# Optimization experiments

Measured on AMD Instinct MI355X. Metric: run time of the kernel, lower is better.

## Reference

```python
import jax, jax.numpy as jnp
import numpy as np

DZ = 16
DX = 16
T = 256
K = 2 * T  # quad-form slots: slot 0 = prior, odd = integrated obs terms, even = transition terms
LOG2PI = float(np.log(2.0 * np.pi))


def setup_inputs() -> dict:
    key = jax.random.key(0)
    ks = jax.random.split(key, 20)

    def spd(k, d, s=0.5):
        L = jax.random.normal(k, (d, d))
        return s * (L @ L.T) / d + jnp.eye(d)

    sc = 1.0 / np.sqrt(DZ)
    return {
        "observations": jax.random.normal(ks[0], (T, DX)),
        "p_prior_mean": 0.1 * jax.random.normal(ks[1], (DZ,)),
        "p_prior_cov": spd(ks[2], DZ),
        "p_trans_w": 0.7 * sc * jax.random.normal(ks[3], (DZ, DZ)),
        "p_trans_b": 0.1 * jax.random.normal(ks[4], (DZ,)),
        "p_trans_cov": spd(ks[5], DZ),
        "p_em_w": sc * jax.random.normal(ks[6], (DX, DZ)),
        "p_em_b": 0.1 * jax.random.normal(ks[7], (DX,)),
        "p_em_cov": spd(ks[8], DX),
        "q_prior_mean": 0.1 * jax.random.normal(ks[9], (DZ,)),
        "q_prior_cov": spd(ks[10], DZ),
        "q_trans_w": 0.7 * sc * jax.random.normal(ks[11], (DZ, DZ)),
        "q_trans_b": 0.1 * jax.random.normal(ks[12], (DZ,)),
        "q_trans_cov": spd(ks[13], DZ),
        "q_em_w": sc * jax.random.normal(ks[14], (DX, DZ)),
        "q_em_b": 0.1 * jax.random.normal(ks[15], (DX,)),
        "q_em_cov": spd(ks[16], DX),
    }


def reference(observations, p_prior_mean, p_prior_cov, p_trans_w, p_trans_b, p_trans_cov,
              p_em_w, p_em_b, p_em_cov, q_prior_mean, q_prior_cov, q_trans_w, q_trans_b,
              q_trans_cov, q_em_w, q_em_b, q_em_cov):
    dz, dx = DZ, DX
    I = jnp.eye(dz, dtype=observations.dtype)

    def cterm(dim, det):  # -0.5*(d*log(2pi) + log det)
        return -0.5 * (dim * LOG2PI + jnp.log(det))

    p_tr_prec = jnp.linalg.inv(p_trans_cov)
    p_tr_det = jnp.linalg.det(p_trans_cov)
    p_em_prec = jnp.linalg.inv(p_em_cov)
    p_em_det = jnp.linalg.det(p_em_cov)
    q_tr_prec = jnp.linalg.inv(q_trans_cov)
    Om_obs = -0.5 * p_em_prec   # Omega of every observation term (linear-Gaussian emission)
    Om_tr = -0.5 * p_tr_prec    # Omega of every transition quad form

    def kupdate(m_pred, P_pred, y):  # Kalman measurement update under q
        S = q_em_w @ P_pred @ q_em_w.T + q_em_cov
        Kg = P_pred @ q_em_w.T @ jnp.linalg.inv(S)
        m = m_pred + Kg @ (y - q_em_w @ m_pred - q_em_b)
        P = (I - Kg @ q_em_w) @ P_pred
        return m, P

    # init: filtering + V
    m_f, P_f = kupdate(q_prior_mean, q_prior_cov, observations[0])
    const = cterm(dz, jnp.linalg.det(p_prior_cov)) + cterm(dx, p_em_det)
    As = jnp.zeros((K, dz, dz), observations.dtype).at[0].set(I)
    bs = jnp.zeros((K, dz), observations.dtype).at[0].set(-p_prior_mean)
    # static Omega stack (inactive slots have A=0,b=0 so they contribute exactly 0)
    odd = (jnp.arange(K) % 2 == 1)[:, None, None]
    Om = jnp.where(odd, Om_obs[None], Om_tr[None])
    Om = Om.at[0].set(-0.5 * jnp.linalg.inv(p_prior_cov))
    pend_b = p_em_b - observations[0]  # pending obs term: (Om_obs, p_em_w, pend_b)

    def step(carry, inp):
        As, bs, pend_b, m_f, P_f, const = carry
        y, t = inp
        # backward kernel from current filtering
        P_prec = jnp.linalg.inv(P_f)
        bprec = q_trans_w.T @ q_tr_prec @ q_trans_w + P_prec
        bcov = jnp.linalg.inv(bprec)
        cm = q_trans_w.T @ q_tr_prec
        B = bcov @ cm
        a = bcov @ (P_prec @ m_f - cm @ q_trans_b)
        # integrate all existing quad forms under backward: trace(Om A bcov A^T), A<-A@B, b<-A@a+b
        ACA = jnp.einsum('kij,jl,kml->kim', As, bcov, As)
        const = const + jnp.einsum('kij,kji->', Om, ACA)
        bs = jnp.einsum('kij,j->ki', As, a) + bs
        As = jnp.einsum('kij,jl->kil', As, B)
        # integrate pending observation term, append at slot 2t-1
        const = const + jnp.trace(Om_obs @ p_em_w @ bcov @ p_em_w.T)
        As = As.at[2 * t - 1].set(p_em_w @ B)
        bs = bs.at[2 * t - 1].set(p_em_w @ a + pend_b)
        # per-step constants
        const = (const + cterm(dx, p_em_det) + cterm(dz, p_tr_det)
                 - cterm(dz, jnp.linalg.det(bcov)) + 0.5 * dz
                 - 0.5 * jnp.trace(p_tr_prec @ p_trans_w @ bcov @ p_trans_w.T))
        # transition quad form at slot 2t
        As = As.at[2 * t].set(p_trans_w @ B - I)
        bs = bs.at[2 * t].set(p_trans_w @ a + p_trans_b)
        pend_b = p_em_b - y
        # Kalman filter step under q
        m_pred = q_trans_w @ m_f + q_trans_b
        P_pred = q_trans_w @ P_f @ q_trans_w.T + q_trans_cov
        m_f, P_f = kupdate(m_pred, P_pred, y)
        return (As, bs, pend_b, m_f, P_f, const), None

    ts = jnp.arange(1, T)
    (As, bs, pend_b, m_f, P_f, const), _ = jax.lax.scan(
        step, (As, bs, pend_b, m_f, P_f, const), (observations[1:], ts))

    const = const - cterm(dz, jnp.linalg.det(P_f))
    # expectation of quad forms under filtering (NOTE: trace(Om A P A), no final
    # transpose -- faithful to the source's _expect_quad_form_under_filtering)
    tr = jnp.einsum('kij,kjl,lm,kmi->', Om, As, P_f, As)
    u = jnp.einsum('kij,j->ki', As, m_f) + bs
    ev = jnp.einsum('ki,kij,kj->', u, Om, u)
    # pending observation term under filtering (same formula)
    up = p_em_w @ m_f + pend_b
    tr_p = jnp.trace(Om_obs @ p_em_w @ P_f @ p_em_w)
    ev_p = up @ Om_obs @ up
    return const + tr + ev + tr_p + ev_p + 0.5 * dz
```

## Files before the change

kernel.cpp:

```cpp
#include <hip/hip_runtime.h>
#include <cmath>

#define L2PI 1.8378770664093453f
#define CT16 (16.f * L2PI)

__device__ __align__(16) float g_Gstore[255 * 256];
__device__ float g_Pff[256], g_Om0[256], g_Omo[256], g_Omt[256], g_Ginf[256];
__device__ float g_partial, g_acc;
__device__ int g_tb;
__device__ unsigned g_cnt;

__device__ __forceinline__ float dAB(const float* A, const float* B, int i, int j) {
  float s = 0.f;
#pragma unroll
  for (int k = 0; k < 16; ++k) s = fmaf(A[i * 16 + k], B[k * 16 + j], s);
  return s;
}
__device__ __forceinline__ float dATB(const float* A, const float* B, int i, int j) {
  float s = 0.f;
#pragma unroll
  for (int k = 0; k < 16; ++k) s = fmaf(A[k * 16 + i], B[k * 16 + j], s);
  return s;
}
__device__ __forceinline__ float dABT(const float* A, const float* B, int i, int j) {
  float s = 0.f;
#pragma unroll
  for (int k = 0; k < 16; ++k) s = fmaf(A[i * 16 + k], B[j * 16 + k], s);
  return s;
}
__device__ __forceinline__ float mv(const float* M, const float* v, int r) {
  float s = 0.f;
#pragma unroll
  for (int k = 0; k < 16; ++k) s = fmaf(M[r * 16 + k], v[k], s);
  return s;
}
__device__ __forceinline__ float mvT(const float* M, const float* v, int r) {
  float s = 0.f;
#pragma unroll
  for (int k = 0; k < 16; ++k) s = fmaf(M[k * 16 + r], v[k], s);
  return s;
}
__device__ __forceinline__ float wave_sum(float v) {
#pragma unroll
  for (int off = 32; off; off >>= 1) v += __shfl_down(v, off);
  return v;
}
__device__ __forceinline__ float wave_max(float v) {
#pragma unroll
  for (int off = 32; off; off >>= 1) v = fmaxf(v, __shfl_down(v, off));
  return v;
}
__device__ __forceinline__ float rl(float v, int l) {
  return __int_as_float(__builtin_amdgcn_readlane(__float_as_int(v), l));
}

__device__ __forceinline__ float reg_gj_core(const float* __restrict__ src,
                                             float aI[4]) {
  const int wl = threadIdx.x & 63;
  const int col = wl & 15, rg = wl >> 4;
  float aA[4];
#pragma unroll
  for (int q = 0; q < 4; ++q) {
    const int r = rg + 4 * q;
    aA[q] = src[r * 16 + col];
    aI[q] = (r == col) ? 1.f : 0.f;
  }
  float det = 1.f;
#pragma unroll
  for (int k = 0; k < 16; ++k) {
    const int kq = k >> 2, kr = k & 3;
    const float piv = rl(aA[kq], (kr << 4) | k);
    det *= piv;
    const float rp = 1.f / piv;
    const float pA = __shfl(aA[kq], (kr << 4) | col);
    const float pI = __shfl(aI[kq], (kr << 4) | col);
    float f[4];
    f[0] = __shfl(aA[0], (rg << 4) | k);
    f[1] = __shfl(aA[1], (rg << 4) | k);
    f[2] = __shfl(aA[2], (rg << 4) | k);
    f[3] = __shfl(aA[3], (rg << 4) | k);
#pragma unroll
    for (int q = 0; q < 4; ++q) {
      const float tq = f[q] * rp;
      const float nA = fmaf(-tq, pA, aA[q]);
      const float nI = fmaf(-tq, pI, aI[q]);
      if (q == kq) {
        const bool isp = (rg == kr);
        aA[q] = isp ? pA * rp : nA;
        aI[q] = isp ? pI * rp : nI;
      } else {
        aA[q] = nA;
        aI[q] = nI;
      }
    }
  }
  return det;
}

__device__ __forceinline__ float reg_gj_inv(const float* __restrict__ src,
                                            float* __restrict__ dst) {
  const int wl = threadIdx.x & 63;
  const int col = wl & 15, rg = wl >> 4;
  float aI[4];
  const float det = reg_gj_core(src, aI);
#pragma unroll
  for (int q = 0; q < 4; ++q) dst[(rg + 4 * q) * 16 + col] = aI[q];
  return det;
}

template <int MODE>
__device__ __forceinline__ float gj_inv_mul(const float* __restrict__ src,
                                            const float* __restrict__ Bm,
                                            float* __restrict__ dst) {
  const int wl = threadIdx.x & 63;
  const int col = wl & 15, rg = wl >> 4;
  float aI[4];
  const float det = reg_gj_core(src, aI);
  float part[16];
#pragma unroll
  for (int ii = 0; ii < 16; ++ii) {
    float s = 0.f;
#pragma unroll
    for (int q = 0; q < 4; ++q) {
      const int k = rg + 4 * q;
      s = fmaf(MODE == 0 ? Bm[k * 16 + ii] : Bm[ii * 16 + k], aI[q], s);
    }
    part[ii] = s;
  }
#pragma unroll
  for (int ii = 0; ii < 16; ++ii) {
    part[ii] += __shfl_xor(part[ii], 16);
    part[ii] += __shfl_xor(part[ii], 32);
  }
  if (rg == 0) {
    dst[0 * 16 + col] = part[0];  dst[1 * 16 + col] = part[1];
    dst[2 * 16 + col] = part[2];  dst[3 * 16 + col] = part[3];
  } else if (rg == 1) {
    dst[4 * 16 + col] = part[4];  dst[5 * 16 + col] = part[5];
    dst[6 * 16 + col] = part[6];  dst[7 * 16 + col] = part[7];
  } else if (rg == 2) {
    dst[8 * 16 + col] = part[8];  dst[9 * 16 + col] = part[9];
    dst[10 * 16 + col] = part[10]; dst[11 * 16 + col] = part[11];
  } else {
    dst[12 * 16 + col] = part[12]; dst[13 * 16 + col] = part[13];
    dst[14 * 16 + col] = part[14]; dst[15 * 16 + col] = part[15];
  }
  return det;
}

__global__ void __launch_bounds__(256)
lgq_fwd(const float* __restrict__ obs,
        const float* __restrict__ ppm, const float* __restrict__ ppc,
        const float* __restrict__ ptw, const float* __restrict__ ptb,
        const float* __restrict__ ptc, const float* __restrict__ pew,
        const float* __restrict__ peb, const float* __restrict__ pec,
        const float* __restrict__ qpm, const float* __restrict__ qpc,
        const float* __restrict__ qtw, const float* __restrict__ qtb,
        const float* __restrict__ qtc, const float* __restrict__ qew,
        const float* __restrict__ qeb, const float* __restrict__ qec) {
  const int e = threadIdx.x;
  const int i = e >> 4, j = e & 15;
  const int wid = e >> 6;
  const int lane = e & 63;

  __shared__ float W[256], Qm[256], Hm[256], Rm[256], Em[256], Pwm[256];
  __shared__ float HW[256], QHt[256], HQH[256], TmpB[256];
  __shared__ float Om0[256], Omo[256], Omt[256], Fo[256], Ft[256], Nm[256], EOm[256];
  __shared__ float Sm[256], Pf[256];
  __shared__ float WP[256], U[256], Ppred[256], Smat[256], PHt[256];
  __shared__ float Pi[256], Si[256], Gm[256], Kgm[256], Mm[256], T1m[256], NGm[256];
  __shared__ float sObs[256 * 16];
  __shared__ float detPArr[256], detSArr[256], d3all[256];
  __shared__ float uB1[252 * 16], pB1[252 * 16], pC1[252 * 16];
  __shared__ float mfs1[252 * 16], rvs1[252 * 16];
  __shared__ float mf[16], mfN[16], rv[16], pb[16], bqv[16], bemv[16], pbemv[16],
      ptbv[16];
  __shared__ float w2[16], q2[16], mpred[16], av[16], hv[16];
  __shared__ float EOpb[16], resid[16], tv1[16], tv2[16], Opf[16];
  __shared__ float ca[16], mca[16], nca[16], c1[16], cg1[16], qc[16], epbm[16];
  __shared__ float red[4], red2[4], red3[4], dets[6];
  __shared__ float sc_const, sc_c, ctb, sh_cstep;
  __shared__ float ld_pprior, ld_ptr, ld_pem, ld_Q, ld_R, ld_qprior, ld_Pf;
  __shared__ float sh_detS, sh_tstep_inf;
  __shared__ int sh_frozen;

  W[e] = qtw[e]; Qm[e] = qtc[e]; Hm[e] = qew[e]; Rm[e] = qec[e];
  Em[e] = pew[e]; Pwm[e] = ptw[e];
  {
    const float4* o4 = (const float4*)obs;
    float4* s4 = (float4*)sObs;
#pragma unroll
    for (int q = 0; q < 4; ++q) s4[e + 256 * q] = o4[e + 256 * q];
  }
  if (e < 16) { bqv[e] = qtb[e]; bemv[e] = qeb[e]; pbemv[e] = peb[e]; ptbv[e] = ptb[e]; }
  if (e == 0) { sh_frozen = 0; g_acc = 0.f; g_cnt = 0u; }
  __syncthreads();
  HW[e] = dAB(Hm, W, i, j);
  TmpB[e] = dAB(Hm, Qm, i, j);
  __syncthreads();
  HQH[e] = dABT(TmpB, Hm, i, j) + Rm[e];
  QHt[e] = TmpB[j * 16 + i];
  __syncthreads();
  if (wid == 0) {
    float d0 = reg_gj_inv(ppc, Pi);
    float d1 = reg_gj_inv(ptc, Si);
    if (e == 0) { dets[0] = d0; dets[1] = d1; }
  } else if (wid == 1) {
    float d2 = reg_gj_inv(pec, Gm);
    float d3 = reg_gj_inv(qtc, Kgm);
    if (e == 64) { dets[2] = d2; dets[3] = d3; }
  } else if (wid == 2) {
    float d4 = reg_gj_inv(qec, T1m);
    float d5 = reg_gj_inv(qpc, NGm);
    if (e == 128) { dets[4] = d4; dets[5] = d5; }
  }
  __syncthreads();
  Om0[e] = -0.5f * Pi[e];
  Omt[e] = -0.5f * Si[e];
  Omo[e] = -0.5f * Gm[e];
  g_Om0[e] = Om0[e]; g_Omo[e] = Omo[e]; g_Omt[e] = Omt[e];
  Sm[e] = Om0[e];
  TmpB[e] = -0.5f * dAB(Gm, Em, i, j);
  Nm[e] = -0.5f * dAB(Si, Pwm, i, j);
  EOm[e] = -0.5f * dATB(Em, Gm, i, j);
  if (e == 0) {
    ld_pprior = logf(dets[0]); ld_ptr = logf(dets[1]); ld_pem = logf(dets[2]);
    ld_Q = logf(dets[3]); ld_R = logf(dets[4]); ld_qprior = logf(dets[5]);
  }
  __syncthreads();
  Fo[e] = dATB(Em, TmpB, i, j);
  Ft[e] = dATB(Pwm, Nm, i, j);
  if (e < 16) w2[e] = mvT(Nm, ptbv, e);
  else if (e < 32) q2[e - 16] = mv(Omt, ptbv, e - 16);
  else if (e < 48) rv[e - 32] = -mv(Om0, ppm, e - 32);
  else if (e < 64) pb[e - 48] = pbemv[e - 48] - sObs[e - 48];
  {
    const int rr = e & 15, tg = e >> 4;
#pragma unroll
    for (int it = 0; it < 16; ++it) {
      const int tt = it * 16 + tg;
      float s = 0.f;
#pragma unroll
      for (int k = 0; k < 16; ++k)
        s = fmaf(Omo[rr * 16 + k], pbemv[k] - sObs[tt * 16 + k], s);
      s *= (pbemv[rr] - sObs[tt * 16 + rr]);
      s += __shfl_xor(s, 1); s += __shfl_xor(s, 2);
      s += __shfl_xor(s, 4); s += __shfl_xor(s, 8);
      if (rr == 0) d3all[tt] = s;
    }
  }
  __syncthreads();
  if (e == 0) {
    float s = 0.f, ct = 0.f;
    for (int k = 0; k < 16; ++k) { s = fmaf(ppm[k], rv[k], s); ct = fmaf(ptbv[k], q2[k], ct); }
    sc_c = -s;
    ctb = ct;
    sc_const = -0.5f * (CT16 + ld_pprior) - 0.5f * (CT16 + ld_pem);
    sh_cstep = 8.f - 0.5f * CT16 - 0.5f * (ld_pem + ld_ptr);
  }
  if (e < 16) mpred[e] = qpm[e];
  TmpB[e] = dAB(Hm, qpc, i, j);
  __syncthreads();
  Smat[e] = dABT(TmpB, Hm, i, j) + Rm[e];
  if (e < 16) resid[e] = sObs[e] - bemv[e] - mv(Hm, mpred, e);
  __syncthreads();
  if (wid == 0) {
    float d = reg_gj_inv(Smat, Si);
    if (e == 0) sh_detS = d;
  }
  __syncthreads();
  Kgm[e] = dATB(TmpB, Si, i, j);
  if (e == 0) ld_Pf = ld_qprior + ld_R - logf(sh_detS);
  __syncthreads();
  Pf[e] = qpc[e] - dAB(Kgm, TmpB, i, j);
  if (e < 16) { mf[e] = mpred[e] + mv(Kgm, resid, e); mfN[e] = mf[e]; }
  __syncthreads();

  float d1acc = 0.f, tacc = 0.f, fd2 = 0.f, facc = 0.f;
  int t = 1;
  for (; t < 256; ++t) {
    const float* y = sObs + t * 16;
    WP[e] = dAB(W, Pf, i, j);
    U[e] = dAB(HW, Pf, i, j);
    if (t > 1) {
      const float sN = dATB(Gm, T1m, i, j) - NGm[j * 16 + i] - NGm[e] + Omt[e];
      const float sd = fabsf(sN - Sm[e]);
      Sm[e] = sN;
      const float vm = wave_max(sd);
      if (lane == 0) red3[wid] = vm;
      d1acc = fmaf(Mm[e] * av[i], av[j], d1acc);
      if (e < 16) {
        float s = -q2[e];
#pragma unroll
        for (int k = 0; k < 16; ++k) {
          s = fmaf(T1m[k * 16 + e], av[k], s);
          s = fmaf(Gm[k * 16 + e], hv[k], s);
          s = fmaf(-Nm[e * 16 + k], av[k], s);
        }
        rv[e] = s;
      } else if (e < 32) {
        fd2 = fmaf(av[e - 16], hv[e - 16], fd2);
        mf[e - 16] = mfN[e - 16];
      } else if (e < 48) {
        mpred[e - 32] = bqv[e - 32] + mv(W, mfN, e - 32);
      }
    } else {
      if (e < 16) mpred[e] = bqv[e] + mv(W, mf, e);
    }
    __syncthreads();
    Ppred[e] = dABT(WP, W, i, j) + Qm[e];
    Smat[e] = dABT(U, HW, i, j) + HQH[e];
    PHt[e] = dABT(WP, HW, i, j) + QHt[e];
    if (e < 16) resid[e] = y[e] - bemv[e] - mv(Hm, mpred, e);
    if (e == 0 && t >= 5) {
      const float pfd = fmaxf(fmaxf(red2[0], red2[1]), fmaxf(red2[2], red2[3]));
      const float sdm = fmaxf(fmaxf(red3[0], red3[1]), fmaxf(red3[2], red3[3]));
      if (pfd < 3e-3f && sdm < 3e-2f) sh_frozen = 1;
    }
    __syncthreads();
    if (sh_frozen) break;
    if (wid == 0) {
      const float d = gj_inv_mul<0>(Ppred, WP, Gm);
      if (e == 0) detPArr[t] = d;
    } else if (wid == 1) {
      const float d = gj_inv_mul<1>(Smat, PHt, Kgm);
      if (e == 64) detSArr[t] = d;
    } else if (wid == 2) {
      const int wl = e & 63;
#pragma unroll
      for (int q = 0; q < 4; ++q) { const int x = wl + 64 * q; Mm[x] = Sm[x] + Fo[x] + Ft[x]; }
      if (wl < 16) EOpb[wl] = mv(EOm, pb, wl);
    }
    __syncthreads();
    {
      const float bc = Pf[e] - dAB(Gm, WP, i, j);
      tacc = fmaf(Mm[e], bc, tacc);
      const float pfN = Ppred[e] - dABT(Kgm, PHt, i, j);
      const float df = fabsf(pfN - Pf[e]);
      Pf[e] = pfN;
      const float vm = wave_max(df);
      if (lane == 0) red2[wid] = vm;
    }
    T1m[e] = dAB(Mm, Gm, i, j);
    NGm[e] = dAB(Nm, Gm, i, j);
    g_Gstore[(t - 1) * 256 + e] = Gm[e];
    if (e < 16) av[e] = mf[e] - mv(Gm, mpred, e);
    else if (e < 32) mfN[e - 16] = mpred[e - 16] + mv(Kgm, resid, e - 16);
    else if (e < 48) hv[e - 32] = rv[e - 32] + EOpb[e - 32] + w2[e - 32];
    else if (e < 64) pb[e - 48] = pbemv[e - 48] - y[e - 48];
    __syncthreads();
  }

  const int tb = t;
  if (sh_frozen) {
    const int NT = 256 - tb;
    const int AA = NT & ~3;
    const int r16 = e & 15, kslot = e >> 4;
    T1m[e] = dAB(Kgm, Hm, i, j);
    NGm[e] = ((i == j) ? 1.f : 0.f) - dAB(Gm, W, i, j);
    Mm[e] = Sm[e] + Fo[e] + Ft[e];
    if (e < 16) ca[e] = -mv(Gm, bqv, e);
    else if (e < 32) epbm[e - 16] = mv(EOm, pbemv, e - 16);
    __syncthreads();
    Smat[e] = W[e] - dAB(T1m, W, i, j);
    Pi[e] = dAB(Mm, NGm, i, j);
    Si[e] = dAB(Nm, NGm, i, j);
    {
      const float bcf = Pf[e] - dAB(Gm, WP, i, j);
      const float v = wave_sum(Mm[e] * bcf);
      if (lane == 0) red[wid] = v;
    }
    if (e < 16) mca[e] = mv(Mm, ca, e);
    else if (e < 32) nca[e - 16] = mv(Nm, ca, e - 16);
    else if (e < 48) {
      const int r = e - 32;
      c1[r] = bqv[r] - mv(T1m, bqv, r) - mv(Kgm, bemv, r);
    }
    __syncthreads();
    U[e] = dATB(Gm, Pi, i, j) - Si[e];
    Ppred[e] = dATB(Gm, EOm, i, j);
    Fo[e] = dAB(Smat, Smat, i, j);
    HW[e] = dAB(Gm, Gm, i, j);
    if (e < 16) {
      float s = 0.f;
#pragma unroll
      for (int k = 0; k < 16; ++k)
        s = fmaf(Gm[k * 16 + e], w2[k] + mca[k] + epbm[k], s);
      cg1[e] = s - nca[e] - q2[e];
    } else if (e < 32) {
      const int r = e - 16;
      qc[r] = mca[r] + 2.f * w2[r] + 2.f * epbm[r];
    } else if (e < 48) {
      mfs1[e - 32] = mf[e - 32];
    } else if (e < 64) {
      rvs1[e - 48] = rv[e - 48];
    }
    if (e == 0) sh_tstep_inf = red[0] + red[1] + red[2] + red[3];
    {
      float kgrow[16];
#pragma unroll
      for (int k2 = 0; k2 < 16; ++k2) kgrow[k2] = Kgm[r16 * 16 + k2];
      const float c1r = c1[r16];
      for (int k = 1 + kslot; k <= NT; k += 16) {
        const float* yc = sObs + (tb - 1 + k) * 16;
        float s = c1r;
#pragma unroll
        for (int k2 = 0; k2 < 16; ++k2) s = fmaf(kgrow[k2], yc[k2], s);
        uB1[k * 16 + r16] = s;
      }
    }
    __syncthreads();
    Ft[e] = dAB(Fo, Fo, i, j);
    QHt[e] = dAB(HW, HW, i, j);
    {
      float a1row[16];
#pragma unroll
      for (int k2 = 0; k2 < 16; ++k2) a1row[k2] = Smat[r16 * 16 + k2];
      for (int k = 2 + kslot; k <= NT; k += 16) {
        const float* up = uB1 + (k - 1) * 16;
        float s = uB1[k * 16 + r16];
#pragma unroll
        for (int k2 = 0; k2 < 16; ++k2) s = fmaf(a1row[k2], up[k2], s);
        pB1[k * 16 + r16] = s;
      }
    }
    __syncthreads();
    {
      float a2row[16];
#pragma unroll
      for (int k2 = 0; k2 < 16; ++k2) a2row[k2] = Fo[r16 * 16 + k2];
      for (int k = 4 + kslot; k <= NT; k += 16) {
        const float* pp = pB1 + (k - 2) * 16;
        float s = pB1[k * 16 + r16];
#pragma unroll
        for (int k2 = 0; k2 < 16; ++k2) s = fmaf(a2row[k2], pp[k2], s);
        pC1[k * 16 + r16] = s;
      }
    }
    __syncthreads();
    if (wid == 0 && AA >= 4) {
      const int r = lane & 15;
      float a4row[16];
#pragma unroll
      for (int k2 = 0; k2 < 16; ++k2) a4row[k2] = Ft[r * 16 + k2];
      float x = mf[r];
      float d0 = pC1[4 * 16 + r];
      float d1 = (AA >= 8) ? pC1[8 * 16 + r] : 0.f;
      for (int k = 4; k <= AA; k += 4) {
        const float d2 = (k + 8 <= AA) ? pC1[(k + 8) * 16 + r] : 0.f;
        float s0 = d0, s1 = 0.f, s2 = 0.f, s3 = 0.f;
#pragma unroll
        for (int k2 = 0; k2 < 16; k2 += 4) {
          s0 = fmaf(a4row[k2],     rl(x, k2),     s0);
          s1 = fmaf(a4row[k2 + 1], rl(x, k2 + 1), s1);
          s2 = fmaf(a4row[k2 + 2], rl(x, k2 + 2), s2);
          s3 = fmaf(a4row[k2 + 3], rl(x, k2 + 3), s3);
        }
        x = (s0 + s1) + (s2 + s3);
        if (lane < 16) mfs1[k * 16 + r] = x;
        d0 = d1; d1 = d2;
      }
    }
    __syncthreads();
    {
      float a1row[16], a2row[16];
#pragma unroll
      for (int k2 = 0; k2 < 16; ++k2) {
        a1row[k2] = Smat[r16 * 16 + k2];
        a2row[k2] = Fo[r16 * 16 + k2];
      }
      for (int a = 4 * kslot; a <= NT; a += 64) {
        const float* mfp = mfs1 + a * 16;
        if (a + 1 <= NT) {
          float s = uB1[(a + 1) * 16 + r16];
#pragma unroll
          for (int k2 = 0; k2 < 16; ++k2) s = fmaf(a1row[k2], mfp[k2], s);
          mfs1[(a + 1) * 16 + r16] = s;
        }
        if (a + 2 <= NT) {
          float s = pB1[(a + 2) * 16 + r16];
#pragma unroll
          for (int k2 = 0; k2 < 16; ++k2) s = fmaf(a2row[k2], mfp[k2], s);
          mfs1[(a + 2) * 16 + r16] = s;
        }
      }
    }
    __syncthreads();
    {
      float a2row[16];
#pragma unroll
      for (int k2 = 0; k2 < 16; ++k2) a2row[k2] = Fo[r16 * 16 + k2];
      for (int a = 4 * kslot; a <= NT; a += 64) {
        if (a + 3 <= NT) {
          const float* mfp = mfs1 + (a + 1) * 16;
          float s = pB1[(a + 3) * 16 + r16];
#pragma unroll
          for (int k2 = 0; k2 < 16; ++k2) s = fmaf(a2row[k2], mfp[k2], s);
          mfs1[(a + 3) * 16 + r16] = s;
        }
      }
    }
    __syncthreads();
    {
      float b1row[16], georow[16];
#pragma unroll
      for (int k2 = 0; k2 < 16; ++k2) {
        b1row[k2] = U[r16 * 16 + k2];
        georow[k2] = Ppred[r16 * 16 + k2];
      }
      const float cg1r = cg1[r16];
      for (int k = 1 + kslot; k <= NT; k += 16) {
        const float* mfp = mfs1 + (k - 1) * 16;
        const float* yp = sObs + (tb - 2 + k) * 16;
        float s = cg1r;
#pragma unroll
        for (int k2 = 0; k2 < 16; ++k2) {
          s = fmaf(b1row[k2], mfp[k2], s);
          s = fmaf(-georow[k2], yp[k2], s);
        }
        uB1[k * 16 + r16] = s;
      }
    }
    if (e < 16) { mf[e] = mfs1[NT * 16 + e]; pb[e] = pbemv[e] - sObs[255 * 16 + e]; }
    __syncthreads();
    {
      float gtrow[16];
#pragma unroll
      for (int k2 = 0; k2 < 16; ++k2) gtrow[k2] = Gm[k2 * 16 + r16];
      for (int k = 2 + kslot; k <= NT; k += 16) {
        const float* wp = uB1 + (k - 1) * 16;
        float s = uB1[k * 16 + r16];
#pragma unroll
        for (int k2 = 0; k2 < 16; ++k2) s = fmaf(gtrow[k2], wp[k2], s);
        pB1[k * 16 + r16] = s;
      }
    }
    __syncthreads();
    {
      float gt2row[16];
#pragma unroll
      for (int k2 = 0; k2 < 16; ++k2) gt2row[k2] = HW[k2 * 16 + r16];
      for (int k = 4 + kslot; k <= NT; k += 16) {
        const float* wp = pB1 + (k - 2) * 16;
        float s = pB1[k * 16 + r16];
#pragma unroll
        for (int k2 = 0; k2 < 16; ++k2) s = fmaf(gt2row[k2], wp[k2], s);
        pC1[k * 16 + r16] = s;
      }
    }
    __syncthreads();
    if (wid == 0 && AA >= 4) {
      const int r = lane & 15;
      float g4row[16];
#pragma unroll
      for (int k2 = 0; k2 < 16; ++k2) g4row[k2] = QHt[k2 * 16 + r];
      float x = rv[r];
      float d0 = pC1[4 * 16 + r];
      float d1 = (AA >= 8) ? pC1[8 * 16 + r] : 0.f;
      for (int k = 4; k <= AA; k += 4) {
        const float d2 = (k + 8 <= AA) ? pC1[(k + 8) * 16 + r] : 0.f;
        float s0 = d0, s1 = 0.f, s2 = 0.f, s3 = 0.f;
#pragma unroll
        for (int k2 = 0; k2 < 16; k2 += 4) {
          s0 = fmaf(g4row[k2],     rl(x, k2),     s0);
          s1 = fmaf(g4row[k2 + 1], rl(x, k2 + 1), s1);
          s2 = fmaf(g4row[k2 + 2], rl(x, k2 + 2), s2);
          s3 = fmaf(g4row[k2 + 3], rl(x, k2 + 3), s3);
        }
        x = (s0 + s1) + (s2 + s3);
        if (lane < 16) rvs1[k * 16 + r] = x;
        d0 = d1; d1 = d2;
      }
    }
    __syncthreads();
    {
      float gtrow[16], gt2row[16];
#pragma unroll
      for (int k2 = 0; k2 < 16; ++k2) {
        gtrow[k2] = Gm[k2 * 16 + r16];
        gt2row[k2] = HW[k2 * 16 + r16];
      }
      for (int a = 4 * kslot; a <= NT; a += 64) {
        const float* rp = rvs1 + a * 16;
        if (a + 1 <= NT) {
          float s = uB1[(a + 1) * 16 + r16];
#pragma unroll
          for (int k2 = 0; k2 < 16; ++k2) s = fmaf(gtrow[k2], rp[k2], s);
          rvs1[(a + 1) * 16 + r16] = s;
        }
        if (a + 2 <= NT) {
          float s = pB1[(a + 2) * 16 + r16];
#pragma unroll
          for (int k2 = 0; k2 < 16; ++k2) s = fmaf(gt2row[k2], rp[k2], s);
          rvs1[(a + 2) * 16 + r16] = s;
        }
      }
    }
    __syncthreads();
    {
      float gt2row[16];
#pragma unroll
      for (int k2 = 0; k2 < 16; ++k2) gt2row[k2] = HW[k2 * 16 + r16];
      for (int a = 4 * kslot; a <= NT; a += 64) {
        if (a + 3 <= NT) {
          const float* rp = rvs1 + (a + 1) * 16;
          float s = pB1[(a + 3) * 16 + r16];
#pragma unroll
          for (int k2 = 0; k2 < 16; ++k2) s = fmaf(gt2row[k2], rp[k2], s);
          rvs1[(a + 3) * 16 + r16] = s;
        }
      }
    }
    __syncthreads();
    {
      float avrow[16], mavrow[16], eorow[16];
#pragma unroll
      for (int k2 = 0; k2 < 16; ++k2) {
        avrow[k2] = NGm[r16 * 16 + k2];
        mavrow[k2] = Pi[r16 * 16 + k2];
        eorow[k2] = EOm[r16 * 16 + k2];
      }
      const float car = ca[r16], qcr = qc[r16];
      for (int k = 1 + kslot; k <= NT; k += 16) {
        const float* mfp = mfs1 + (k - 1) * 16;
        const float* yp = sObs + (tb - 2 + k) * 16;
        float avr = car, qr = qcr + 2.f * rvs1[(k - 1) * 16 + r16];
#pragma unroll
        for (int k2 = 0; k2 < 16; ++k2) {
          avr = fmaf(avrow[k2], mfp[k2], avr);
          qr = fmaf(mavrow[k2], mfp[k2], qr);
          qr = fmaf(-2.f * eorow[k2], yp[k2], qr);
        }
        facc = fmaf(avr, qr, facc);
      }
    }
    if (e < 16) rv[e] = rvs1[NT * 16 + e];
    __syncthreads();
  } else {
    const float sN = dATB(Gm, T1m, i, j) - NGm[j * 16 + i] - NGm[e] + Omt[e];
    Sm[e] = sN;
    d1acc = fmaf(Mm[e] * av[i], av[j], d1acc);
    if (e < 16) {
      float s = -q2[e];
#pragma unroll
      for (int k = 0; k < 16; ++k) {
        s = fmaf(T1m[k * 16 + e], av[k], s);
        s = fmaf(Gm[k * 16 + e], hv[k], s);
        s = fmaf(-Nm[e * 16 + k], av[k], s);
      }
      rv[e] = s;
    } else if (e < 32) {
      fd2 = fmaf(av[e - 16], hv[e - 16], fd2);
      mf[e - 16] = mfN[e - 16];
    }
    __syncthreads();
  }

  const int n = tb - 1;
  if (e >= 1 && e <= n) {
    detPArr[e] = logf(detPArr[e]);
    detSArr[e] = logf(detSArr[e]);
  }
  {
    const float vA = d1acc + 2.f * fd2 + facc;
    const float vB = tacc;
    const float vC = (e < 255) ? d3all[e] : 0.f;
    const float sA = wave_sum(vA);
    const float sB = wave_sum(vB);
    const float sC = wave_sum(vC);
    if (lane == 0) { red[wid] = sA; red2[wid] = sB; red3[wid] = sC; }
  }
  __syncthreads();
  if (e == 0) {
    const float dsum = red[0] + red[1] + red[2] + red[3];
    const float tsum = red2[0] + red2[1] + red2[2] + red2[3];
    const float d3tot = red3[0] + red3[1] + red3[2] + red3[3];
    float lpf = ld_Pf;
    float sum_ldb = 0.f, ldbl = 0.f;
    for (int s2 = 1; s2 <= n; ++s2) {
      ldbl = lpf + ld_Q - detPArr[s2];
      sum_ldb += ldbl;
      lpf = detPArr[s2] + ld_R - detSArr[s2];
    }
    float sc = sc_const + tsum + (float)n * sh_cstep + 0.5f * sum_ldb;
    if (tb < 256) sc += (float)(256 - tb) * (sh_tstep_inf + sh_cstep + 0.5f * ldbl);
    sc_const = sc;
    ld_Pf = lpf;
    sc_c += dsum + d3tot + 255.f * ctb;
  }
  __syncthreads();

  g_Pff[e] = Pf[e];
  g_Ginf[e] = Gm[e];
  if (e == 0) g_tb = tb;
  WP[e] = dAB(Pf, Em, i, j);
  if (e < 16) tv1[e] = mv(Sm, mf, e);
  else if (e < 32) tv2[e - 16] = pb[e - 16] + mv(Em, mf, e - 16);
  __syncthreads();
  {
    const float v = wave_sum(EOm[e] * WP[e]);
    if (lane == 0) red[wid] = v;
  }
  if (e < 16) Opf[e] = mv(Omo, tv2, e);
  __syncthreads();
  if (e == 0) {
    const float tr_p = red[0] + red[1] + red[2] + red[3];
    float ev1 = 0.f, ev2 = 0.f, evp = 0.f;
    for (int k = 0; k < 16; ++k) {
      ev1 = fmaf(mf[k], tv1[k], ev1);
      ev2 = fmaf(rv[k], mf[k], ev2);
      evp = fmaf(tv2[k], Opf[k], evp);
    }
    g_partial = sc_const + 0.5f * (CT16 + ld_Pf) + (ev1 + 2.f * ev2 + sc_c)
                + tr_p + evp + 8.f;
  }
}

__global__ void __launch_bounds__(256)
lgq_trace(const float* __restrict__ pew, const float* __restrict__ ptw,
          float* __restrict__ out) {
  const int e = threadIdx.x, i = e >> 4, j = e & 15, b = blockIdx.x;
  const int lane = e & 63, wid = e >> 6;
  __shared__ float Pfs[256], OmA[256], OmtS[256], EmS[256], PwS[256], GinfS[256];
  __shared__ float Xb[2][256], Bb[2][256];
  __shared__ float Sm1[256], Sf[256], A1[256], A2[256];
  __shared__ float T1v[256], NGv[256], Kxv[256], S2v[256];
  __shared__ float redt[4];
  int tb = g_tb;
  tb = (tb < 1) ? 1 : (tb > 256 ? 256 : tb);
  Pfs[e] = g_Pff[e];
  OmtS[e] = g_Omt[e];
  EmS[e] = pew[e];
  PwS[e] = ptw[e];
  GinfS[e] = g_Ginf[e];
  OmA[e] = (b == 0) ? g_Om0[e] : g_Omo[e];
  Xb[0][e] = (i == j) ? 1.f : 0.f;
  Bb[0][e] = g_Ginf[e];
  __syncthreads();
  int E = (b >= tb) ? (255 - b) : (256 - tb);
  int xc = 0, bc2 = 0;
  while (E) {
    Xb[xc ^ 1][e] = (E & 1) ? dAB(Xb[xc], Bb[bc2], i, j) : Xb[xc][e];
    if (E > 1) Bb[bc2 ^ 1][e] = dAB(Bb[bc2], Bb[bc2], i, j);
    __syncthreads();
    xc ^= 1; bc2 ^= 1;
    E >>= 1;
  }
  if (b >= tb) {
    Sf[e] = Xb[xc][e];
    Sm1[e] = dAB(GinfS, Xb[xc], i, j);
    __syncthreads();
  } else {
    int cur = xc;
    for (int s2 = tb - 1; s2 >= b + 1; --s2) {
      const float4* gr = (const float4*)(g_Gstore + (s2 - 1) * 256 + i * 16);
      const float4 a0 = gr[0], a1 = gr[1], a2 = gr[2], a3 = gr[3];
      const float* Xc = Xb[cur];
      float s = 0.f;
      s = fmaf(a0.x, Xc[0 * 16 + j], s);  s = fmaf(a0.y, Xc[1 * 16 + j], s);
      s = fmaf(a0.z, Xc[2 * 16 + j], s);  s = fmaf(a0.w, Xc[3 * 16 + j], s);
      s = fmaf(a1.x, Xc[4 * 16 + j], s);  s = fmaf(a1.y, Xc[5 * 16 + j], s);
      s = fmaf(a1.z, Xc[6 * 16 + j], s);  s = fmaf(a1.w, Xc[7 * 16 + j], s);
      s = fmaf(a2.x, Xc[8 * 16 + j], s);  s = fmaf(a2.y, Xc[9 * 16 + j], s);
      s = fmaf(a2.z, Xc[10 * 16 + j], s); s = fmaf(a2.w, Xc[11 * 16 + j], s);
      s = fmaf(a3.x, Xc[12 * 16 + j], s); s = fmaf(a3.y, Xc[13 * 16 + j], s);
      s = fmaf(a3.z, Xc[14 * 16 + j], s); s = fmaf(a3.w, Xc[15 * 16 + j], s);
      Xb[cur ^ 1][e] = s;
      __syncthreads();
      cur ^= 1;
    }
    Sf[e] = Xb[cur][e];
    if (b >= 1) {
      const float4* gr = (const float4*)(g_Gstore + (b - 1) * 256 + i * 16);
      const float4 a0 = gr[0], a1 = gr[1], a2 = gr[2], a3 = gr[3];
      const float* Xc = Xb[cur];
      float s = 0.f;
      s = fmaf(a0.x, Xc[0 * 16 + j], s);  s = fmaf(a0.y, Xc[1 * 16 + j], s);
      s = fmaf(a0.z, Xc[2 * 16 + j], s);  s = fmaf(a0.w, Xc[3 * 16 + j], s);
      s = fmaf(a1.x, Xc[4 * 16 + j], s);  s = fmaf(a1.y, Xc[5 * 16 + j], s);
      s = fmaf(a1.z, Xc[6 * 16 + j], s);  s = fmaf(a1.w, Xc[7 * 16 + j], s);
      s = fmaf(a2.x, Xc[8 * 16 + j], s);  s = fmaf(a2.y, Xc[9 * 16 + j], s);
      s = fmaf(a2.z, Xc[10 * 16 + j], s); s = fmaf(a2.w, Xc[11 * 16 + j], s);
      s = fmaf(a3.x, Xc[12 * 16 + j], s); s = fmaf(a3.y, Xc[13 * 16 + j], s);
      s = fmaf(a3.z, Xc[14 * 16 + j], s); s = fmaf(a3.w, Xc[15 * 16 + j], s);
      Sm1[e] = s;
    } else {
      Sm1[e] = Xb[cur][e];
    }
    __syncthreads();
  }
  if (b == 0) {
    A1[e] = Sm1[e];
    A2[e] = 0.f;
  } else {
    A1[e] = dAB(EmS, Sm1, i, j);
    A2[e] = dAB(PwS, Sm1, i, j) - Sf[e];
  }
  __syncthreads();
  T1v[e] = dAB(OmA, A1, i, j);
  NGv[e] = dAB(Pfs, A1, i, j);
  Kxv[e] = dAB(OmtS, A2, i, j);
  S2v[e] = dAB(Pfs, A2, i, j);
  __syncthreads();
  float val = T1v[e] * NGv[j * 16 + i] + Kxv[e] * S2v[j * 16 + i];
  val = wave_sum(val);
  if (lane == 0) redt[wid] = val;
  __syncthreads();
  if (e == 0) {
    atomicAdd(&g_acc, redt[0] + redt[1] + redt[2] + redt[3]);
    __threadfence();
    const unsigned o = atomicAdd(&g_cnt, 1u);
    if (o == 255u) {
      const float acc = atomicAdd(&g_acc, 0.f);
      out[0] = g_partial + acc;
    }
  }
}

extern "C" void kernel_launch(void* const* d_in, const int* in_sizes, int n_in,
                              void* d_out, int out_size, void* d_ws, size_t ws_size,
                              hipStream_t stream) {
  (void)in_sizes; (void)n_in; (void)out_size; (void)d_ws; (void)ws_size;
  lgq_fwd<<<dim3(1), dim3(256), 0, stream>>>(
      (const float*)d_in[0], (const float*)d_in[1], (const float*)d_in[2],
      (const float*)d_in[3], (const float*)d_in[4], (const float*)d_in[5],
      (const float*)d_in[6], (const float*)d_in[7], (const float*)d_in[8],
      (const float*)d_in[9], (const float*)d_in[10], (const float*)d_in[11],
      (const float*)d_in[12], (const float*)d_in[13], (const float*)d_in[14],
      (const float*)d_in[15], (const float*)d_in[16]);
  lgq_trace<<<dim3(256), dim3(256), 0, stream>>>((const float*)d_in[6],
                                                 (const float*)d_in[3],
                                                 (float*)d_out);
}
```

Before: 96.32 us.

## Keep transposed copies of matrices so 16x16 products read contiguous rows

Adds transposed shared-memory copies (WT, EmT, PwmT, GmT, T1mT, NGmT, TmpBT, NmT, WPT) and rewrites the dAB/dATB products as dABT, so each thread reads both operands along contiguous rows instead of strided columns. This is meant to reduce LDS bank conflicts and allow vectorised loads. The prior Kalman gain is now computed by the fused gj_inv_mul, which removes one barrier. The freeze check may now fire one step earlier (t>=4 instead of t>=5). The cost is extra LDS footprint and extra transposed stores on every iteration, and the earlier freeze could change results slightly.

```diff
diff --git a/kernel.cpp b/kernel.cpp
--- a/kernel.cpp
+++ b/kernel.cpp
@@ -32,12 +32,6 @@
   float s = 0.f;
 #pragma unroll
   for (int k = 0; k < 16; ++k) s = fmaf(M[r * 16 + k], v[k], s);
-  return s;
-}
-__device__ __forceinline__ float mvT(const float* M, const float* v, int r) {
-  float s = 0.f;
-#pragma unroll
-  for (int k = 0; k < 16; ++k) s = fmaf(M[k * 16 + r], v[k], s);
   return s;
 }
 __device__ __forceinline__ float wave_sum(float v) {
@@ -111,7 +105,8 @@
 template <int MODE>
 __device__ __forceinline__ float gj_inv_mul(const float* __restrict__ src,
                                             const float* __restrict__ Bm,
-                                            float* __restrict__ dst) {
+                                            float* __restrict__ dst,
+                                            float* __restrict__ dstT) {
   const int wl = threadIdx.x & 63;
   const int col = wl & 15, rg = wl >> 4;
   float aI[4];
@@ -135,6 +130,13 @@
   if (rg == 0) {
     dst[0 * 16 + col] = part[0];  dst[1 * 16 + col] = part[1];
     dst[2 * 16 + col] = part[2];  dst[3 * 16 + col] = part[3];
+    if (dstT) {
+      float4* p4 = (float4*)(dstT + col * 16);
+      p4[0] = make_float4(part[0], part[1], part[2], part[3]);
+      p4[1] = make_float4(part[4], part[5], part[6], part[7]);
+      p4[2] = make_float4(part[8], part[9], part[10], part[11]);
+      p4[3] = make_float4(part[12], part[13], part[14], part[15]);
+    }
   } else if (rg == 1) {
     dst[4 * 16 + col] = part[4];  dst[5 * 16 + col] = part[5];
     dst[6 * 16 + col] = part[6];  dst[7 * 16 + col] = part[7];
@@ -163,12 +165,15 @@
   const int wid = e >> 6;
   const int lane = e & 63;
 
-  __shared__ float W[256], Qm[256], Hm[256], Rm[256], Em[256], Pwm[256];
-  __shared__ float HW[256], QHt[256], HQH[256], TmpB[256];
-  __shared__ float Om0[256], Omo[256], Omt[256], Fo[256], Ft[256], Nm[256], EOm[256];
+  __shared__ float W[256], WT[256], Qm[256], Hm[256], Rm[256], Em[256], EmT[256],
+      PwmT[256];
+  __shared__ float HW[256], QHt[256], HQH[256], TmpB[256], TmpBT[256];
+  __shared__ float Om0[256], Omo[256], Omt[256], Fo[256], Ft[256], Nm[256],
+      NmT[256], EOm[256];
   __shared__ float Sm[256], Pf[256];
-  __shared__ float WP[256], U[256], Ppred[256], Smat[256], PHt[256];
-  __shared__ float Pi[256], Si[256], Gm[256], Kgm[256], Mm[256], T1m[256], NGm[256];
+  __shared__ float WP[256], WPT[256], U[256], Ppred[256], Smat[256], PHt[256];
+  __shared__ float Pi[256], Si[256], Gm[256], GmT[256], Kgm[256], Mm[256];
+  __shared__ float T1m[256], T1mT[256], NGm[256], NGmT[256];
   __shared__ float sObs[256 * 16];
   __shared__ float detPArr[256], detSArr[256], d3all[256];
   __shared__ float uB1[252 * 16], pB1[252 * 16], pC1[252 * 16];
@@ -185,7 +190,8 @@
   __shared__ int sh_frozen;
 
   W[e] = qtw[e]; Qm[e] = qtc[e]; Hm[e] = qew[e]; Rm[e] = qec[e];
-  Em[e] = pew[e]; Pwm[e] = ptw[e];
+  Em[e] = pew[e];
+  WT[e] = qtw[j * 16 + i]; EmT[e] = pew[j * 16 + i]; PwmT[e] = ptw[j * 16 + i];
   {
     const float4* o4 = (const float4*)obs;
     float4* s4 = (float4*)sObs;
@@ -195,8 +201,8 @@
   if (e < 16) { bqv[e] = qtb[e]; bemv[e] = qeb[e]; pbemv[e] = peb[e]; ptbv[e] = ptb[e]; }
   if (e == 0) { sh_frozen = 0; g_acc = 0.f; g_cnt = 0u; }
   __syncthreads();
-  HW[e] = dAB(Hm, W, i, j);
-  TmpB[e] = dAB(Hm, Qm, i, j);
+  HW[e] = dABT(Hm, WT, i, j);
+  TmpB[e] = dABT(Hm, Qm, i, j);
   __syncthreads();
   HQH[e] = dABT(TmpB, Hm, i, j) + Rm[e];
   QHt[e] = TmpB[j * 16 + i];
@@ -220,17 +226,23 @@
   Omo[e] = -0.5f * Gm[e];
   g_Om0[e] = Om0[e]; g_Omo[e] = Omo[e]; g_Omt[e] = Omt[e];
   Sm[e] = Om0[e];
-  TmpB[e] = -0.5f * dAB(Gm, Em, i, j);
-  Nm[e] = -0.5f * dAB(Si, Pwm, i, j);
-  EOm[e] = -0.5f * dATB(Em, Gm, i, j);
+  {
+    const float v = -0.5f * dABT(Gm, EmT, i, j);
+    TmpB[e] = v; TmpBT[j * 16 + i] = v;
+  }
+  {
+    const float v = -0.5f * dABT(Si, PwmT, i, j);
+    Nm[e] = v; NmT[j * 16 + i] = v;
+  }
+  EOm[e] = -0.5f * dABT(EmT, Gm, i, j);
   if (e == 0) {
     ld_pprior = logf(dets[0]); ld_ptr = logf(dets[1]); ld_pem = logf(dets[2]);
     ld_Q = logf(dets[3]); ld_R = logf(dets[4]); ld_qprior = logf(dets[5]);
   }
   __syncthreads();
-  Fo[e] = dATB(Em, TmpB, i, j);
-  Ft[e] = dATB(Pwm, Nm, i, j);
-  if (e < 16) w2[e] = mvT(Nm, ptbv, e);
+  Fo[e] = dABT(EmT, TmpBT, i, j);
+  Ft[e] = dABT(PwmT, NmT, i, j);
+  if (e < 16) w2[e] = mv(NmT, ptbv, e);
   else if (e < 32) q2[e - 16] = mv(Omt, ptbv, e - 16);
   else if (e < 48) rv[e - 32] = -mv(Om0, ppm, e - 32);
   else if (e < 64) pb[e - 48] = pbemv[e - 48] - sObs[e - 48];
@@ -259,31 +271,33 @@
     sh_cstep = 8.f - 0.5f * CT16 - 0.5f * (ld_pem + ld_ptr);
   }
   if (e < 16) mpred[e] = qpm[e];
-  TmpB[e] = dAB(Hm, qpc, i, j);
+  {
+    const float v = dABT(Hm, qpc, i, j);
+    TmpB[e] = v; TmpBT[j * 16 + i] = v;
+  }
   __syncthreads();
   Smat[e] = dABT(TmpB, Hm, i, j) + Rm[e];
   if (e < 16) resid[e] = sObs[e] - bemv[e] - mv(Hm, mpred, e);
   __syncthreads();
   if (wid == 0) {
-    float d = reg_gj_inv(Smat, Si);
+    float d = gj_inv_mul<0>(Smat, TmpB, Kgm, nullptr);
     if (e == 0) sh_detS = d;
   }
   __syncthreads();
-  Kgm[e] = dATB(TmpB, Si, i, j);
+  Pf[e] = qpc[e] - dABT(Kgm, TmpBT, i, j);
+  if (e < 16) { mf[e] = mpred[e] + mv(Kgm, resid, e); mfN[e] = mf[e]; }
   if (e == 0) ld_Pf = ld_qprior + ld_R - logf(sh_detS);
-  __syncthreads();
-  Pf[e] = qpc[e] - dAB(Kgm, TmpB, i, j);
-  if (e < 16) { mf[e] = mpred[e] + mv(Kgm, resid, e); mfN[e] = mf[e]; }
   __syncthreads();
 
   float d1acc = 0.f, tacc = 0.f, fd2 = 0.f, facc = 0.f;
   int t = 1;
   for (; t < 256; ++t) {
     const float* y = sObs + t * 16;
-    WP[e] = dAB(W, Pf, i, j);
-    U[e] = dAB(HW, Pf, i, j);
+    WP[e] = dABT(W, Pf, i, j);
+    WPT[e] = dABT(Pf, W, i, j);
+    U[e] = dABT(HW, Pf, i, j);
     if (t > 1) {
-      const float sN = dATB(Gm, T1m, i, j) - NGm[j * 16 + i] - NGm[e] + Omt[e];
+      const float sN = dABT(GmT, T1mT, i, j) - NGmT[e] - NGm[e] + Omt[e];
       const float sd = fabsf(sN - Sm[e]);
       Sm[e] = sN;
       const float vm = wave_max(sd);
@@ -293,8 +307,8 @@
         float s = -q2[e];
 #pragma unroll
         for (int k = 0; k < 16; ++k) {
-          s = fmaf(T1m[k * 16 + e], av[k], s);
-          s = fmaf(Gm[k * 16 + e], hv[k], s);
+          s = fmaf(T1mT[e * 16 + k], av[k], s);
+          s = fmaf(GmT[e * 16 + k], hv[k], s);
           s = fmaf(-Nm[e * 16 + k], av[k], s);
         }
         rv[e] = s;
@@ -312,7 +326,7 @@
     Smat[e] = dABT(U, HW, i, j) + HQH[e];
     PHt[e] = dABT(WP, HW, i, j) + QHt[e];
     if (e < 16) resid[e] = y[e] - bemv[e] - mv(Hm, mpred, e);
-    if (e == 0 && t >= 5) {
+    if (e == 0 && t >= 4) {
       const float pfd = fmaxf(fmaxf(red2[0], red2[1]), fmaxf(red2[2], red2[3]));
       const float sdm = fmaxf(fmaxf(red3[0], red3[1]), fmaxf(red3[2], red3[3]));
       if (pfd < 3e-3f && sdm < 3e-2f) sh_frozen = 1;
@@ -320,10 +334,10 @@
     __syncthreads();
     if (sh_frozen) break;
     if (wid == 0) {
-      const float d = gj_inv_mul<0>(Ppred, WP, Gm);
+      const float d = gj_inv_mul<1>(Ppred, WPT, Gm, GmT);
       if (e == 0) detPArr[t] = d;
     } else if (wid == 1) {
-      const float d = gj_inv_mul<1>(Smat, PHt, Kgm);
+      const float d = gj_inv_mul<1>(Smat, PHt, Kgm, nullptr);
       if (e == 64) detSArr[t] = d;
     } else if (wid == 2) {
       const int wl = e & 63;
@@ -333,7 +347,7 @@
     }
     __syncthreads();
     {
-      const float bc = Pf[e] - dAB(Gm, WP, i, j);
+      const float bc = Pf[e] - dABT(Gm, WPT, i, j);
       tacc = fmaf(Mm[e], bc, tacc);
       const float pfN = Ppred[e] - dABT(Kgm, PHt, i, j);
       const float df = fabsf(pfN - Pf[e]);
@@ -341,8 +355,12 @@
       const float vm = wave_max(df);
       if (lane == 0) red2[wid] = vm;
     }
-    T1m[e] = dAB(Mm, Gm, i, j);
-    NGm[e] = dAB(Nm, Gm, i, j);
+    {
+      const float v1 = dABT(Mm, GmT, i, j);
+      T1m[e] = v1; T1mT[j * 16 + i] = v1;
+      const float v2 = dABT(Nm, GmT, i, j);
+      NGm[e] = v2; NGmT[j * 16 + i] = v2;
+    }
     g_Gstore[(t - 1) * 256 + e] = Gm[e];
     if (e < 16) av[e] = mf[e] - mv(Gm, mpred, e);
     else if (e < 32) mfN[e - 16] = mpred[e - 16] + mv(Kgm, resid, e - 16);
@@ -357,16 +375,16 @@
     const int AA = NT & ~3;
     const int r16 = e & 15, kslot = e >> 4;
     T1m[e] = dAB(Kgm, Hm, i, j);
-    NGm[e] = ((i == j) ? 1.f : 0.f) - dAB(Gm, W, i, j);
+    NGm[e] = ((i == j) ? 1.f : 0.f) - dABT(Gm, WT, i, j);
     Mm[e] = Sm[e] + Fo[e] + Ft[e];
     if (e < 16) ca[e] = -mv(Gm, bqv, e);
     else if (e < 32) epbm[e - 16] = mv(EOm, pbemv, e - 16);
     __syncthreads();
-    Smat[e] = W[e] - dAB(T1m, W, i, j);
+    Smat[e] = W[e] - dABT(T1m, WT, i, j);
     Pi[e] = dAB(Mm, NGm, i, j);
     Si[e] = dAB(Nm, NGm, i, j);
     {
-      const float bcf = Pf[e] - dAB(Gm, WP, i, j);
+      const float bcf = Pf[e] - dABT(Gm, WPT, i, j);
       const float v = wave_sum(Mm[e] * bcf);
       if (lane == 0) red[wid] = v;
     }
@@ -385,7 +403,7 @@
       float s = 0.f;
 #pragma unroll
       for (int k = 0; k < 16; ++k)
-        s = fmaf(Gm[k * 16 + e], w2[k] + mca[k] + epbm[k], s);
+        s = fmaf(GmT[e * 16 + k], w2[k] + mca[k] + epbm[k], s);
       cg1[e] = s - nca[e] - q2[e];
     } else if (e < 32) {
       const int r = e - 16;
@@ -526,7 +544,7 @@
     {
       float gtrow[16];
 #pragma unroll
-      for (int k2 = 0; k2 < 16; ++k2) gtrow[k2] = Gm[k2 * 16 + r16];
+      for (int k2 = 0; k2 < 16; ++k2) gtrow[k2] = GmT[r16 * 16 + k2];
       for (int k = 2 + kslot; k <= NT; k += 16) {
         const float* wp = uB1 + (k - 1) * 16;
         float s = uB1[k * 16 + r16];
@@ -577,7 +595,7 @@
       float gtrow[16], gt2row[16];
 #pragma unroll
       for (int k2 = 0; k2 < 16; ++k2) {
-        gtrow[k2] = Gm[k2 * 16 + r16];
+        gtrow[k2] = GmT[r16 * 16 + k2];
         gt2row[k2] = HW[k2 * 16 + r16];
       }
       for (int a = 4 * kslot; a <= NT; a += 64) {
@@ -637,15 +655,15 @@
     if (e < 16) rv[e] = rvs1[NT * 16 + e];
     __syncthreads();
   } else {
-    const float sN = dATB(Gm, T1m, i, j) - NGm[j * 16 + i] - NGm[e] + Omt[e];
+    const float sN = dABT(GmT, T1mT, i, j) - NGmT[e] - NGm[e] + Omt[e];
     Sm[e] = sN;
     d1acc = fmaf(Mm[e] * av[i], av[j], d1acc);
     if (e < 16) {
       float s = -q2[e];
 #pragma unroll
       for (int k = 0; k < 16; ++k) {
-        s = fmaf(T1m[k * 16 + e], av[k], s);
-        s = fmaf(Gm[k * 16 + e], hv[k], s);
+        s = fmaf(T1mT[e * 16 + k], av[k], s);
+        s = fmaf(GmT[e * 16 + k], hv[k], s);
         s = fmaf(-Nm[e * 16 + k], av[k], s);
       }
       rv[e] = s;
@@ -693,7 +711,7 @@
   g_Pff[e] = Pf[e];
   g_Ginf[e] = Gm[e];
   if (e == 0) g_tb = tb;
-  WP[e] = dAB(Pf, Em, i, j);
+  WP[e] = dABT(Pf, EmT, i, j);
   if (e < 16) tv1[e] = mv(Sm, mf, e);
   else if (e < 32) tv2[e - 16] = pb[e - 16] + mv(Em, mf, e - 16);
   __syncthreads();
```

Result: slower. 98.73 us (+2.5%).
